# Optimization experiments

Measured on AMD Instinct MI355X. Metric: run time of the kernel, lower is better.

The kernel has to match this reference:

```python
import jax, jax.numpy as jnp
import numpy as np

N = 50000
E = 600000
D = 128


def gcn_conv(x, row, col, w, W, b):
    """PyG GCNConv: add self-loops (weight 1), symmetric deg^-1/2 normalization,
    linear transform, edge-weighted scatter-add aggregation, then bias."""
    n = x.shape[0]
    loop = jnp.arange(n)
    r = jnp.concatenate([row, loop])            # source nodes, [E+N]
    c = jnp.concatenate([col, loop])            # target nodes, [E+N]
    ww = jnp.concatenate([w, jnp.ones((n,), x.dtype)])
    deg = jax.ops.segment_sum(ww, c, num_segments=n)          # weighted in-degree
    dinv = jnp.where(deg > 0, jax.lax.rsqrt(deg), jnp.zeros_like(deg))
    norm = dinv[r] * ww * dinv[c]               # [E+N]
    xl = x @ W                                  # [n, D_out]
    msg = norm[:, None] * xl[r]                 # gather + scale, [E+N, D_out]
    out = jax.ops.segment_sum(msg, c, num_segments=n)
    return out + b


def setup_inputs() -> dict:
    key = jax.random.key(0)
    ks = jax.random.split(key, 12)
    x = jax.random.normal(ks[0], (N, D), dtype=jnp.float32)
    edge_index = jax.random.randint(ks[1], (2, E), 0, N, dtype=jnp.int64)
    edge_weights = jax.random.uniform(ks[2], (E,), dtype=jnp.float32)
    s = 1.0 / np.sqrt(D)
    W1 = jax.random.uniform(ks[3], (D, D), jnp.float32, -s, s)
    b1 = jnp.zeros((D,), jnp.float32)
    W2 = jax.random.uniform(ks[4], (D, D), jnp.float32, -s, s)
    b2 = jnp.zeros((D,), jnp.float32)
    W3 = jax.random.uniform(ks[5], (D, D), jnp.float32, -s, s)
    b3 = jnp.zeros((D,), jnp.float32)
    prelu_w = jnp.array(0.25, jnp.float32)
    return {"x": x, "edge_index": edge_index, "edge_weights": edge_weights,
            "W1": W1, "b1": b1, "W2": W2, "b2": b2, "W3": W3, "b3": b3,
            "prelu_w": prelu_w}


def reference(x, edge_index, edge_weights, W1, b1, W2, b2, W3, b3, prelu_w):
    row, col = edge_index[0], edge_index[1]
    # layer 1: GCNConv -> (dropout: eval, identity) -> ELU
    h = gcn_conv(x, row, col, edge_weights, W1, b1)
    h = jax.nn.elu(h)
    # layer 2: GCNConv -> GELU (torch default = exact erf)
    h = gcn_conv(h, row, col, edge_weights, W2, b2)
    h = jax.nn.gelu(h, approximate=False)
    # layer 3: GCNConv -> PReLU (learnable scalar slope)
    h = gcn_conv(h, row, col, edge_weights, W3, b3)
    h = jnp.where(h >= 0, h, prelu_w * h)
    return h
```

## Files before the change

### kernel.cpp

```cpp
#include <hip/hip_runtime.h>
#include <hip/hip_fp16.h>
#include <math.h>

constexpr int D = 128;
constexpr int CAPC = 1024;

struct __align__(16) H8 { __half2 h[4]; };

typedef _Float16     half8   __attribute__((ext_vector_type(8)));
typedef float        floatx4 __attribute__((ext_vector_type(4)));
typedef unsigned int uint4v  __attribute__((ext_vector_type(4)));
typedef unsigned int uint2v  __attribute__((ext_vector_type(2)));


__device__ __forceinline__ int detect64(const int* __restrict__ ei) {
  int z = 0;
#pragma unroll
  for (int i = 0; i < 8; ++i) z |= ei[2 * i + 1];
  return (z == 0) ? 1 : 0;
}

__device__ __forceinline__ void load_edge(const int* __restrict__ ei, int e, int nE,
                                          int m64, int n, int& r, int& c) {
  if (m64) { r = ei[2 * (size_t)e]; c = ei[2 * ((size_t)nE + e)]; }
  else     { r = ei[(size_t)e];     c = ei[(size_t)nE + e]; }
  r = min(max(r, 0), n - 1);
  c = min(max(c, 0), n - 1);
}

__global__ void k_setup(const float* __restrict__ W1, const float* __restrict__ W2,
                        const float* __restrict__ W3, __half* __restrict__ Wt,
                        unsigned long long* __restrict__ cntdeg, int n8) {
  int b = blockIdx.x;
  if (b < 24) {
    int m = b >> 3, s = b & 7;
    const float* W = m == 0 ? W1 : (m == 1 ? W2 : W3);
    __half* o = Wt + (size_t)m * D * D;
    int t = threadIdx.x;
    int nn = t & 127;
    int kh = t >> 7;
    int k0 = s * 16 + kh * 8;
    H8 hv;
#pragma unroll
    for (int jj = 0; jj < 4; ++jj) {
      float f0 = W[(size_t)(k0 + 2 * jj)     * D + nn];
      float f1 = W[(size_t)(k0 + 2 * jj + 1) * D + nn];
      hv.h[jj] = __floats2half2_rn(f0, f1);
    }
    *(H8*)(o + (size_t)nn * D + k0) = hv;
  } else {
    int i = (b - 24) * 256 + threadIdx.x;
    if (i < n8) cntdeg[i] = 0ULL;
  }
}

template <int ACT>
__device__ __forceinline__ float act_f(float x) {
  if (ACT == 1) return x > 0.f ? x : expm1f(x);
  if (ACT == 2) return 0.5f * x * (1.0f + erff(x * 0.70710678118654752440f));
  return x;
}

__device__ __forceinline__ void gemm_body(int bid, const float* __restrict__ A,
                                          const __half* __restrict__ Wt,
                                          __half* __restrict__ Y, int n) {
  const int wave = threadIdx.x >> 6;
  const int lane = threadIdx.x & 63;
  const int np = lane & 15;
  const int quad = lane >> 4;
  const int node = bid * 64 + wave * 16 + np;
  const int nc = min(node, n - 1);

  half8 b[4];
#pragma unroll
  for (int s = 0; s < 4; ++s) {
    const float* ap = A + (size_t)nc * D + s * 32 + quad * 8;
    floatx4 v0 = __builtin_nontemporal_load((const floatx4*)ap);
    floatx4 v1 = __builtin_nontemporal_load((const floatx4*)(ap + 4));
#pragma unroll
    for (int t = 0; t < 4; ++t) {
      b[s][t]     = (_Float16)v0[t];
      b[s][t + 4] = (_Float16)v1[t];
    }
  }

  floatx4 acc[8];
#pragma unroll
  for (int mt = 0; mt < 8; ++mt) acc[mt] = (floatx4){0.f, 0.f, 0.f, 0.f};

#pragma unroll
  for (int mt = 0; mt < 8; ++mt) {
#pragma unroll
    for (int s = 0; s < 4; ++s) {
      half8 a = *(const half8*)(Wt + (size_t)(mt * 16 + np) * D + s * 32 + quad * 8);
      acc[mt] = __builtin_amdgcn_mfma_f32_16x16x32_f16(a, b[s], acc[mt], 0, 0, 0);
    }
  }

  if (node < n) {
#pragma unroll
    for (int mt = 0; mt < 8; ++mt) {
      __half2 ha = __floats2half2_rn(acc[mt][0], acc[mt][1]);
      __half2 hb = __floats2half2_rn(acc[mt][2], acc[mt][3]);
      uint2v pv;
      pv[0] = *(unsigned int*)&ha;
      pv[1] = *(unsigned int*)&hb;
      int f0 = mt * 16 + quad * 4;
      __builtin_nontemporal_store(
          pv, (uint2v*)(Y + ((size_t)(f0 >> 5) * n + node) * 32 + (f0 & 31)));
    }
  }
}

__global__ __launch_bounds__(256) void k_gemmh(const __half* __restrict__ A,
                                               const __half* __restrict__ Wt,
                                               __half* __restrict__ Y, int n) {
  const int wave = threadIdx.x >> 6;
  const int lane = threadIdx.x & 63;
  const int np = lane & 15;
  const int quad = lane >> 4;
  const int node = blockIdx.x * 64 + wave * 16 + np;
  const int nc = min(node, n - 1);

  half8 b[4];
#pragma unroll
  for (int s = 0; s < 4; ++s)
    b[s] = __builtin_nontemporal_load(
        (const half8*)(A + ((size_t)s * n + nc) * 32 + quad * 8));

  floatx4 acc[8];
#pragma unroll
  for (int mt = 0; mt < 8; ++mt) acc[mt] = (floatx4){0.f, 0.f, 0.f, 0.f};

#pragma unroll
  for (int mt = 0; mt < 8; ++mt) {
#pragma unroll
    for (int s = 0; s < 4; ++s) {
      half8 a = *(const half8*)(Wt + (size_t)(mt * 16 + np) * D + s * 32 + quad * 8);
      acc[mt] = __builtin_amdgcn_mfma_f32_16x16x32_f16(a, b[s], acc[mt], 0, 0, 0);
    }
  }

  if (node < n) {
#pragma unroll
    for (int mt = 0; mt < 8; ++mt) {
      __half2 ha = __floats2half2_rn(acc[mt][0], acc[mt][1]);
      __half2 hb = __floats2half2_rn(acc[mt][2], acc[mt][3]);
      uint2v pv;
      pv[0] = *(unsigned int*)&ha;
      pv[1] = *(unsigned int*)&hb;
      int f0 = mt * 16 + quad * 4;
      __builtin_nontemporal_store(
          pv, (uint2v*)(Y + ((size_t)(f0 >> 5) * n + node) * 32 + (f0 & 31)));
    }
  }
}

__global__ __launch_bounds__(256) void k_posgemm(const float* __restrict__ x,
                                                 const __half* __restrict__ Wt,
                                                 __half* __restrict__ Y,
                                                 const int* __restrict__ ei,
                                                 const float* __restrict__ w,
                                                 unsigned long long* __restrict__ cntdeg,
                                                 int2* __restrict__ rc,
                                                 int* __restrict__ pos,
                                                 int nE, int n, int gb) {
  int b = blockIdx.x;
  if (b < gb) {
    gemm_body(b, x, Wt, Y, n);
    return;
  }
  int e = (b - gb) * blockDim.x + threadIdx.x;
  if (e >= nE) return;
  int m64 = detect64(ei);
  int r, c;
  load_edge(ei, e, nE, m64, n, r, c);
  rc[e] = make_int2(r, c);
  float wf = fminf(fmaxf(w[e], 0.0f), 65535.0f);
  unsigned long long pk =
      (1ULL << 32) | (unsigned long long)__float2uint_rn(wf * 65536.0f);
  unsigned long long old = atomicAdd(&cntdeg[(size_t)c << 3], pk);
  pos[e] = (int)(old >> 32);
}

__global__ void k_scan1(const unsigned long long* __restrict__ cntdeg,
                        int* __restrict__ offs, int* __restrict__ bsum, int n) {
  __shared__ int s[256];
  int t = threadIdx.x;
  int i = blockIdx.x * 256 + t;
  int v = 0;
  if (i < n) {
    int cn = (int)(cntdeg[(size_t)i << 3] >> 32);
    v = (cn + 3) & ~3;
  }
  s[t] = v;
  __syncthreads();
  for (int off = 1; off < 256; off <<= 1) {
    int x = 0;
    if (t >= off) x = s[t - off];
    __syncthreads();
    if (t >= off) s[t] += x;
    __syncthreads();
  }
  if (i < n) offs[i] = s[t] - v;
  if (t == 255) bsum[blockIdx.x] = s[255];
}

__global__ void k_scan23(int* __restrict__ offs, const int* __restrict__ bsum,
                         const unsigned long long* __restrict__ cntdeg,
                         float* __restrict__ dinv, int n, int nb) {
  __shared__ int s[256];
  int t = threadIdx.x;
  int v = (t < nb) ? bsum[t] : 0;
  s[t] = v;
  __syncthreads();
  for (int off = 1; off < 256; off <<= 1) {
    int x = 0;
    if (t >= off) x = s[t - off];
    __syncthreads();
    if (t >= off) s[t] += x;
    __syncthreads();
  }
  int b = blockIdx.x;
  int boffb = (b == 0) ? 0 : s[b - 1];
  int i = b * 256 + t;
  if (i < n) {
    offs[i] += boffb;
    float degf =
        (float)(unsigned int)(cntdeg[(size_t)i << 3] & 0xffffffffULL) * (1.0f / 65536.0f);
    dinv[i] = rsqrtf(1.0f + degf);
  }
  if (i == 0) offs[n] = s[nb - 1];
}

__global__ void k_fill(const int2* __restrict__ rc, const int* __restrict__ pos,
                       const float* __restrict__ w, const int* __restrict__ offs,
                       const unsigned long long* __restrict__ cntdeg,
                       const float* __restrict__ dinv,
                       unsigned int* __restrict__ ecf2, int nE, int n) {
  int e = blockIdx.x * blockDim.x + threadIdx.x;
  if (e < nE) {
    int2 p = rc[e];
    int idx = offs[p.y] + pos[e];
    float cf = dinv[p.x] * w[e];
    ecf2[idx] = ((unsigned int)p.x << 16) |
                (unsigned int)__half_as_ushort(__float2half_rn(cf));
  }
  if (e < n) {
    int q0 = offs[e] + (int)(cntdeg[(size_t)e << 3] >> 32), q1 = offs[e + 1];
    for (int q = q0; q < q1; ++q) ecf2[q] = 0;
  }
}

__device__ __forceinline__ void fmacc8(float* acc, float c, const H8& y) {
  const _Float16* hp = (const _Float16*)&y;
#pragma unroll
  for (int i = 0; i < 8; ++i) acc[i] = fmaf(c, (float)hp[i], acc[i]);
}

__device__ __forceinline__ float cdecode(unsigned int u) {
  return __half2float(__ushort_as_half((unsigned short)(u & 0xffffu)));
}

__device__ __forceinline__ void gather4(H8* y, uint4v u, const __half* __restrict__ Yc,
                                        int j) {
#pragma unroll
  for (int i = 0; i < 4; ++i)
    y[i] = *(const H8*)(Yc + (size_t)(u[i] >> 16) * 32 + j * 8);
}

__device__ __forceinline__ void accum4(float* acc, uint4v u, const H8* y) {
#pragma unroll
  for (int i = 0; i < 4; ++i) fmacc8(acc, cdecode(u[i]), y[i]);
}

#define LDC(p) (((p) - seg_lo + 4 <= CAPC) ? *(const uint4v*)&sc[(p) - seg_lo] \
                                           : *(const uint4v*)(ecf2 + (p)))

template <int ACT, int PRELU, typename OutT>
__global__ __launch_bounds__(256) void k_agg(const __half* __restrict__ Yin,
                                             const int* __restrict__ offs,
                                             const unsigned int* __restrict__ ecf2,
                                             const float* __restrict__ dinv,
                                             const float* __restrict__ bias,
                                             const float* __restrict__ pw,
                                             OutT* __restrict__ OUT, int n) {
  __shared__ unsigned int sc[CAPC];
  __shared__ int soff[33];
  const int chunk = blockIdx.x & 3;
  const int t = threadIdx.x;
  const int node0 = (blockIdx.x >> 2) * 32;
  const int nl = t >> 3;
  const int node = node0 + nl;
  const int sub = (t >> 2) & 1;
  const int j = t & 3;

  const int seg_lo = offs[node0];
  const int seg_hi = offs[min(node0 + 32, n)];
  const int segN = min(seg_hi - seg_lo, CAPC);
  for (int i = t * 4; i < segN; i += 1024)
    *(uint4v*)&sc[i] =
        __builtin_nontemporal_load((const uint4v*)(ecf2 + seg_lo + i));
  if (t < 33) soff[t] = offs[min(node0 + t, n)];
  __syncthreads();

  const __half* Yc = Yin + (size_t)chunk * n * 32;
  const int ncl = min(node, n - 1);
  float dc = dinv[ncl];
  float acc[8] = {0.f, 0.f, 0.f, 0.f, 0.f, 0.f, 0.f, 0.f};

  H8 ys{};
  if (sub == 0) ys = *(const H8*)(Yc + (size_t)ncl * 32 + j * 8);

  int lo = soff[nl], hi = soff[nl + 1];
  int nb4 = (hi - lo) >> 2;
  int em = lo + (((nb4 + 1) >> 1) << 2);
  int b0 = sub ? em : lo;
  int be = sub ? hi : em;
  if (b0 < be) {
    uint4v u0, u1;
    H8 y0[4], y1[4];
    u0 = LDC(b0);
    gather4(y0, u0, Yc, j);
    if (b0 + 4 < be) { u1 = LDC(b0 + 4); gather4(y1, u1, Yc, j); }
    int b = b0;
    while (true) {
      accum4(acc, u0, y0);
      if (b + 8 < be) { u0 = LDC(b + 8); gather4(y0, u0, Yc, j); }
      b += 4; if (b >= be) break;
      accum4(acc, u1, y1);
      if (b + 8 < be) { u1 = LDC(b + 8); gather4(y1, u1, Yc, j); }
      b += 4; if (b >= be) break;
    }
  }
  if (sub == 0) fmacc8(acc, dc, ys);

#pragma unroll
  for (int i = 0; i < 8; ++i) acc[i] += __shfl_xor(acc[i], 4, 64);

  if (sub == 0 && node < n) {
    floatx4 ba = *(const floatx4*)(bias + chunk * 32 + j * 8);
    floatx4 bb = *(const floatx4*)(bias + chunk * 32 + j * 8 + 4);
    float o[8];
#pragma unroll
    for (int i = 0; i < 8; ++i)
      o[i] = act_f<ACT>(dc * acc[i] + (i < 4 ? ba[i] : bb[i - 4]));
    if (PRELU) {
      float wv = *pw;
#pragma unroll
      for (int i = 0; i < 8; ++i) o[i] = o[i] >= 0.f ? o[i] : wv * o[i];
    }
    if constexpr (sizeof(OutT) == 4) {
      floatx4 v0 = {o[0], o[1], o[2], o[3]};
      floatx4 v1 = {o[4], o[5], o[6], o[7]};
      float* op = (float*)OUT + (size_t)node * D + chunk * 32 + j * 8;
      __builtin_nontemporal_store(v0, (floatx4*)op);
      __builtin_nontemporal_store(v1, (floatx4*)(op + 4));
    } else {
      H8 hw;
#pragma unroll
      for (int i = 0; i < 4; ++i) hw.h[i] = __floats2half2_rn(o[2 * i], o[2 * i + 1]);
      __builtin_nontemporal_store(
          *(uint4v*)&hw,
          (uint4v*)((__half*)OUT + ((size_t)chunk * n + node) * 32 + j * 8));
    }
  }
}

extern "C" void kernel_launch(void* const* d_in, const int* in_sizes, int n_in,
                              void* d_out, int out_size, void* d_ws, size_t ws_size,
                              hipStream_t stream) {
  const float* x  = (const float*)d_in[0];
  const int*   ei = (const int*)d_in[1];
  const float* w  = (const float*)d_in[2];
  const float* W1 = (const float*)d_in[3];
  const float* b1 = (const float*)d_in[4];
  const float* W2 = (const float*)d_in[5];
  const float* b2 = (const float*)d_in[6];
  const float* W3 = (const float*)d_in[7];
  const float* b3 = (const float*)d_in[8];
  const float* pw = (const float*)d_in[9];
  const int N = in_sizes[0] / D;
  const int E = in_sizes[2];
  float* out = (float*)d_out;

  char* wsb = (char*)d_ws;
  size_t off = 0;
  auto alloc = [&](size_t bytes) {
    void* p = wsb + off;
    off = (off + bytes + 255) & ~(size_t)255;
    return p;
  };
  float*              dinv   = (float*)alloc((size_t)N * 4);
  unsigned long long* cntdeg = (unsigned long long*)alloc((size_t)N * 64);
  int*                offs   = (int*)alloc((size_t)(N + 1) * 4);
  int*                bsum   = (int*)alloc(256 * 4);
  unsigned int*       ecf2   = (unsigned int*)alloc(((size_t)E + 3 * (size_t)N + 64) * 4);
  __half*             Wt     = (__half*)alloc((size_t)3 * D * D * 2);
  __half*             Ya     = (__half*)alloc((size_t)N * D * 2);
  __half*             Yb     = (__half*)alloc((size_t)N * D * 2);
  __half*             h      = (__half*)alloc((size_t)N * D * 2);
  int2*               rc     = (int2*)alloc((size_t)E * 8);
  int*                pos    = (int*)alloc((size_t)E * 4);

  const int nbN = (N + 255) / 256;
  const int eb  = (E + 255) / 256;
  const int fb  = ((E > N ? E : N) + 255) / 256;
  const int n8  = N * 8;
  const int zb  = (n8 + 255) / 256;
  const int gb  = (N + 63) / 64;
  const int ab  = 4 * ((N + 31) / 32);

  hipLaunchKernelGGL(k_setup,   dim3(24 + zb), dim3(256), 0, stream, W1, W2, W3, Wt, cntdeg, n8);
  hipLaunchKernelGGL(k_posgemm, dim3(gb + eb), dim3(256), 0, stream, x, Wt, Ya, ei, w, cntdeg,
                     rc, pos, E, N, gb);
  hipLaunchKernelGGL(k_scan1,   dim3(nbN), dim3(256), 0, stream, cntdeg, offs, bsum, N);
  hipLaunchKernelGGL(k_scan23,  dim3(nbN), dim3(256), 0, stream, offs, bsum, cntdeg, dinv, N, nbN);
  hipLaunchKernelGGL(k_fill,    dim3(fb),  dim3(256), 0, stream, rc, pos, w, offs, cntdeg, dinv, ecf2, E, N);

  hipLaunchKernelGGL((k_agg<1, 0, __half>), dim3(ab), dim3(256), 0, stream, Ya, offs, ecf2, dinv, b1, pw, h, N);
  hipLaunchKernelGGL(k_gemmh,               dim3(gb), dim3(256), 0, stream, h, Wt + D * D,     Yb, N);
  hipLaunchKernelGGL((k_agg<2, 0, __half>), dim3(ab), dim3(256), 0, stream, Yb, offs, ecf2, dinv, b2, pw, h, N);
  hipLaunchKernelGGL(k_gemmh,               dim3(gb), dim3(256), 0, stream, h, Wt + 2 * D * D, Ya, N);
  hipLaunchKernelGGL((k_agg<0, 1, float>),  dim3(ab), dim3(256), 0, stream, Ya, offs, ecf2, dinv, b3, pw, out, N);
}
```

Before: 283.4 us.

## Balance aggregation work across threads via flat edge-quad split and shared atomics

The aggregation kernel stops assigning each node's edges to a fixed pair of threads. Instead it splits the block's whole 32-node edge segment evenly into quads across 64 thread groups, using a per-quad node map, and flushes partial sums into a shared-memory accumulator with atomics when the node changes. This targets load imbalance from skewed node degrees. A separate epilogue then applies the self-loop, bias and activation per node. The edge staging buffer is doubled in size, which raises LDS use per block, and shared atomics plus an extra barrier add overhead.

```diff
diff --git a/kernel.cpp b/kernel.cpp
--- a/kernel.cpp
+++ b/kernel.cpp
@@ -3,7 +3,8 @@
 #include <math.h>
 
 constexpr int D = 128;
-constexpr int CAPC = 1024;
+constexpr int CAPC = 2048;
+constexpr int CAPQ = CAPC / 4;
 
 struct __align__(16) H8 { __half2 h[4]; };
 
@@ -252,12 +253,6 @@
   }
 }
 
-__device__ __forceinline__ void fmacc8(float* acc, float c, const H8& y) {
-  const _Float16* hp = (const _Float16*)&y;
-#pragma unroll
-  for (int i = 0; i < 8; ++i) acc[i] = fmaf(c, (float)hp[i], acc[i]);
-}
-
 __device__ __forceinline__ float cdecode(unsigned int u) {
   return __half2float(__ushort_as_half((unsigned short)(u & 0xffffu)));
 }
@@ -269,13 +264,15 @@
     y[i] = *(const H8*)(Yc + (size_t)(u[i] >> 16) * 32 + j * 8);
 }
 
-__device__ __forceinline__ void accum4(float* acc, uint4v u, const H8* y) {
-#pragma unroll
-  for (int i = 0; i < 4; ++i) fmacc8(acc, cdecode(u[i]), y[i]);
-}
-
-#define LDC(p) (((p) - seg_lo + 4 <= CAPC) ? *(const uint4v*)&sc[(p) - seg_lo] \
-                                           : *(const uint4v*)(ecf2 + (p)))
+__device__ __forceinline__ void accum4p(float* p, uint4v u, const H8* y) {
+#pragma unroll
+  for (int i = 0; i < 4; ++i) {
+    float c = cdecode(u[i]);
+    const _Float16* hp = (const _Float16*)&y[i];
+#pragma unroll
+    for (int k = 0; k < 8; ++k) p[k] = fmaf(c, (float)hp[k], p[k]);
+  }
+}
 
 template <int ACT, int PRELU, typename OutT>
 __global__ __launch_bounds__(256) void k_agg(const __half* __restrict__ Yin,
@@ -285,19 +282,20 @@
                                              const float* __restrict__ bias,
                                              const float* __restrict__ pw,
                                              OutT* __restrict__ OUT, int n) {
+  __shared__ float facc[32][33];
   __shared__ unsigned int sc[CAPC];
   __shared__ int soff[33];
+  __shared__ unsigned char qnode[CAPQ];
   const int chunk = blockIdx.x & 3;
   const int t = threadIdx.x;
   const int node0 = (blockIdx.x >> 2) * 32;
-  const int nl = t >> 3;
-  const int node = node0 + nl;
-  const int sub = (t >> 2) & 1;
-  const int j = t & 3;
-
+  if (node0 >= n) return;
+
+  for (int i = t; i < 32 * 33; i += 256) ((float*)facc)[i] = 0.f;
   const int seg_lo = offs[node0];
   const int seg_hi = offs[min(node0 + 32, n)];
-  const int segN = min(seg_hi - seg_lo, CAPC);
+  const int seg_len = seg_hi - seg_lo;
+  const int segN = min(seg_len, CAPC);
   for (int i = t * 4; i < segN; i += 1024)
     *(uint4v*)&sc[i] =
         __builtin_nontemporal_load((const uint4v*)(ecf2 + seg_lo + i));
@@ -305,64 +303,113 @@
   __syncthreads();
 
   const __half* Yc = Yin + (size_t)chunk * n * 32;
-  const int ncl = min(node, n - 1);
-  float dc = dinv[ncl];
-  float acc[8] = {0.f, 0.f, 0.f, 0.f, 0.f, 0.f, 0.f, 0.f};
-
-  H8 ys{};
-  if (sub == 0) ys = *(const H8*)(Yc + (size_t)ncl * 32 + j * 8);
-
-  int lo = soff[nl], hi = soff[nl + 1];
-  int nb4 = (hi - lo) >> 2;
-  int em = lo + (((nb4 + 1) >> 1) << 2);
-  int b0 = sub ? em : lo;
-  int be = sub ? hi : em;
-  if (b0 < be) {
+  const int j = t & 3;
+
+  if (seg_len <= CAPC) {
+    if (t < 32) {
+      int a = (soff[t] - seg_lo) >> 2, b = (soff[t + 1] - seg_lo) >> 2;
+      for (int q = a; q < b; ++q) qnode[q] = (unsigned char)t;
+    }
+    __syncthreads();
+
+    const int Q = seg_len >> 2;
+    const int g = t >> 2;
+    const int Qp = (Q + 63) >> 6;
+    int q = g * Qp;
+    const int q1 = min(Q, q + Qp);
+
+    float p[8] = {0.f, 0.f, 0.f, 0.f, 0.f, 0.f, 0.f, 0.f};
+    int curn = -1;
     uint4v u0, u1;
     H8 y0[4], y1[4];
-    u0 = LDC(b0);
-    gather4(y0, u0, Yc, j);
-    if (b0 + 4 < be) { u1 = LDC(b0 + 4); gather4(y1, u1, Yc, j); }
-    int b = b0;
-    while (true) {
-      accum4(acc, u0, y0);
-      if (b + 8 < be) { u0 = LDC(b + 8); gather4(y0, u0, Yc, j); }
-      b += 4; if (b >= be) break;
-      accum4(acc, u1, y1);
-      if (b + 8 < be) { u1 = LDC(b + 8); gather4(y1, u1, Yc, j); }
-      b += 4; if (b >= be) break;
-    }
-  }
-  if (sub == 0) fmacc8(acc, dc, ys);
-
-#pragma unroll
-  for (int i = 0; i < 8; ++i) acc[i] += __shfl_xor(acc[i], 4, 64);
-
-  if (sub == 0 && node < n) {
-    floatx4 ba = *(const floatx4*)(bias + chunk * 32 + j * 8);
-    floatx4 bb = *(const floatx4*)(bias + chunk * 32 + j * 8 + 4);
-    float o[8];
-#pragma unroll
-    for (int i = 0; i < 8; ++i)
-      o[i] = act_f<ACT>(dc * acc[i] + (i < 4 ? ba[i] : bb[i - 4]));
+    if (q < q1)     { u0 = *(const uint4v*)&sc[4 * q];       gather4(y0, u0, Yc, j); }
+    if (q + 1 < q1) { u1 = *(const uint4v*)&sc[4 * (q + 1)]; gather4(y1, u1, Yc, j); }
+    while (q < q1) {
+      {
+        int nl = qnode[q];
+        if (nl != curn) {
+          if (curn >= 0) {
+#pragma unroll
+            for (int i = 0; i < 8; ++i) { atomicAdd(&facc[curn][j * 8 + i], p[i]); p[i] = 0.f; }
+          }
+          curn = nl;
+        }
+        accum4p(p, u0, y0);
+        if (q + 2 < q1) { u0 = *(const uint4v*)&sc[4 * (q + 2)]; gather4(y0, u0, Yc, j); }
+      }
+      ++q; if (q >= q1) break;
+      {
+        int nl = qnode[q];
+        if (nl != curn) {
+          if (curn >= 0) {
+#pragma unroll
+            for (int i = 0; i < 8; ++i) { atomicAdd(&facc[curn][j * 8 + i], p[i]); p[i] = 0.f; }
+          }
+          curn = nl;
+        }
+        accum4p(p, u1, y1);
+        if (q + 2 < q1) { u1 = *(const uint4v*)&sc[4 * (q + 2)]; gather4(y1, u1, Yc, j); }
+      }
+      ++q;
+    }
+    if (curn >= 0) {
+#pragma unroll
+      for (int i = 0; i < 8; ++i) atomicAdd(&facc[curn][j * 8 + i], p[i]);
+    }
+  } else {
+    const int nl = t >> 3;
+    const int sub = (t >> 2) & 1;
+    int lo = soff[nl], hi = soff[nl + 1];
+    int nb4 = (hi - lo) >> 2;
+    int em = lo + (((nb4 + 1) >> 1) << 2);
+    int b = sub ? em : lo;
+    int be = sub ? hi : em;
+    float p[8] = {0.f, 0.f, 0.f, 0.f, 0.f, 0.f, 0.f, 0.f};
+    for (; b < be; b += 4) {
+      uint4v u = *(const uint4v*)(ecf2 + b);
+      H8 y[4];
+      gather4(y, u, Yc, j);
+      accum4p(p, u, y);
+    }
+#pragma unroll
+    for (int i = 0; i < 8; ++i) atomicAdd(&facc[nl][j * 8 + i], p[i]);
+  }
+  __syncthreads();
+
+  const int nl2 = t >> 3;
+  const int node2 = node0 + nl2;
+  const int sl = t & 7;
+  if (node2 < n) {
+    float dc = dinv[node2];
+    float dd = dc * dc;
+    const __half2* sp = (const __half2*)(Yc + (size_t)node2 * 32 + sl * 4);
+    float2 f0 = __half22float2(sp[0]);
+    float2 f1 = __half22float2(sp[1]);
+    float selfv[4] = {f0.x, f0.y, f1.x, f1.y};
+    float o[4];
+#pragma unroll
+    for (int i = 0; i < 4; ++i) {
+      float fv = facc[nl2][sl * 4 + i];
+      float bv = bias[chunk * 32 + sl * 4 + i];
+      o[i] = act_f<ACT>(fmaf(dc, fv, fmaf(dd, selfv[i], bv)));
+    }
     if (PRELU) {
       float wv = *pw;
 #pragma unroll
-      for (int i = 0; i < 8; ++i) o[i] = o[i] >= 0.f ? o[i] : wv * o[i];
+      for (int i = 0; i < 4; ++i) o[i] = o[i] >= 0.f ? o[i] : wv * o[i];
     }
     if constexpr (sizeof(OutT) == 4) {
-      floatx4 v0 = {o[0], o[1], o[2], o[3]};
-      floatx4 v1 = {o[4], o[5], o[6], o[7]};
-      float* op = (float*)OUT + (size_t)node * D + chunk * 32 + j * 8;
-      __builtin_nontemporal_store(v0, (floatx4*)op);
-      __builtin_nontemporal_store(v1, (floatx4*)(op + 4));
+      floatx4 v = {o[0], o[1], o[2], o[3]};
+      __builtin_nontemporal_store(
+          v, (floatx4*)((float*)OUT + (size_t)node2 * D + chunk * 32 + sl * 4));
     } else {
-      H8 hw;
-#pragma unroll
-      for (int i = 0; i < 4; ++i) hw.h[i] = __floats2half2_rn(o[2 * i], o[2 * i + 1]);
+      __half2 ha = __floats2half2_rn(o[0], o[1]);
+      __half2 hb = __floats2half2_rn(o[2], o[3]);
+      uint2v pv;
+      pv[0] = *(unsigned int*)&ha;
+      pv[1] = *(unsigned int*)&hb;
       __builtin_nontemporal_store(
-          *(uint4v*)&hw,
-          (uint4v*)((__half*)OUT + ((size_t)chunk * n + node) * 32 + j * 8));
+          pv, (uint2v*)((__half*)OUT + ((size_t)chunk * n + node2) * 32 + sl * 4));
     }
   }
 }
```

Result: slower. 447.6 us (+57.9%).
